# Optimization experiments

Measured on AMD Instinct MI355X. Metric: run time of the kernel, lower is better.

Reference implementation:

```python
import jax, jax.numpy as jnp
import numpy as np

HEADS = 4
K = 3  # neighborhood kernel size
EPS = 1e-5


def _nbr_idx(dim, k):
    # NATTEN semantics: window start clamped so the full k-window stays in-bounds.
    i = jnp.arange(dim)
    start = jnp.clip(i - k // 2, 0, dim - k)
    return start[:, None] + jnp.arange(k)[None, :]  # [dim, k]


def _gather_windows(t, ix, iy, iz):
    # t: [B, X, Y, Z, n, c] -> [B, X, Y, Z, K^3, n, c]
    t = t[:, ix]                 # [B, X, k, Y, Z, n, c]
    t = t[:, :, :, iy]           # [B, X, k, Y, k, Z, n, c]
    t = t[:, :, :, :, :, iz]     # [B, X, k, Y, k, Z, k, n, c]
    t = t.transpose(0, 1, 3, 5, 2, 4, 6, 7, 8)  # [B,X,Y,Z,k,k,k,n,c]
    B, X, Y, Z = t.shape[0], t.shape[1], t.shape[2], t.shape[3]
    return t.reshape(B, X, Y, Z, K * K * K, HEADS, -1)


def setup_inputs() -> dict:
    key = jax.random.key(0)
    k1, k2, k3 = jax.random.split(key, 3)
    C = 128
    x = jax.random.normal(k1, (1, C, 32, 32, 32), dtype=jnp.float32)
    ln_gamma = jnp.ones((C,), jnp.float32)
    ln_beta = jnp.zeros((C,), jnp.float32)
    qkv_w = jax.random.normal(k2, (3 * C, C), dtype=jnp.float32) * 0.02
    qkv_b = jnp.zeros((3 * C,), jnp.float32)
    proj_w = jax.random.normal(k3, (C, C), dtype=jnp.float32) * 0.02
    proj_b = jnp.zeros((C,), jnp.float32)
    return {"x": x, "ln_gamma": ln_gamma, "ln_beta": ln_beta,
            "qkv_w": qkv_w, "qkv_b": qkv_b, "proj_w": proj_w, "proj_b": proj_b}


def reference(x, ln_gamma, ln_beta, qkv_w, qkv_b, proj_w, proj_b):
    B, C, X, Y, Z = x.shape
    hd = C // HEADS
    scale = hd ** -0.5

    # permute to channels-last + LayerNorm over C
    h = x.transpose(0, 2, 3, 4, 1)  # [B,X,Y,Z,C]
    mu = jnp.mean(h, axis=-1, keepdims=True)
    var = jnp.mean(jnp.square(h - mu), axis=-1, keepdims=True)
    h = (h - mu) * jax.lax.rsqrt(var + EPS) * ln_gamma + ln_beta

    # QKV projection
    qkv = h @ qkv_w.T + qkv_b                     # [B,X,Y,Z,3C]
    q, k, v = jnp.split(qkv, 3, axis=-1)
    q = q.reshape(B, X, Y, Z, HEADS, hd)
    k = k.reshape(B, X, Y, Z, HEADS, hd)
    v = v.reshape(B, X, Y, Z, HEADS, hd)

    ix, iy, iz = _nbr_idx(X, K), _nbr_idx(Y, K), _nbr_idx(Z, K)
    k_win = _gather_windows(k, ix, iy, iz)  # [B,X,Y,Z,27,n,hd]
    v_win = _gather_windows(v, ix, iy, iz)

    attn = jnp.einsum('bxyznc,bxyzknc->bxyznk', q * scale, k_win)
    attn = jax.nn.softmax(attn, axis=-1)
    out = jnp.einsum('bxyznk,bxyzknc->bxyznc', attn, v_win)
    out = out.reshape(B, X, Y, Z, C)

    out = out @ proj_w.T + proj_b                 # output projection
    return out.transpose(0, 4, 1, 2, 3) + x      # residual, channels-first
```

## Files before the change

### kernel.cpp

```cpp
#include <hip/hip_runtime.h>

#define N_VOX 32768
#define CCH 128
#define EPSV 1e-5f

typedef __attribute__((ext_vector_type(8))) short bfrag;
typedef __attribute__((ext_vector_type(4))) float ffrag;
typedef __attribute__((ext_vector_type(2))) unsigned int u32x2;

__device__ __forceinline__ float bf2f(unsigned short u) {
    union { unsigned int i; float f; } c; c.i = ((unsigned int)u) << 16; return c.f;
}
__device__ __forceinline__ unsigned short f2bf(float f) {
    union { float f; unsigned int i; } c; c.f = f;
    unsigned int i = c.i;
    return (unsigned short)((i + 0x7FFFu + ((i >> 16) & 1u)) >> 16);
}
__device__ __forceinline__ unsigned int cvtpk(float lo, float hi) {
    unsigned int r;
    asm("v_cvt_pk_bf16_f32 %0, %1, %2" : "=v"(r) : "v"(lo), "v"(hi));
    return r;
}

__global__ __launch_bounds__(256) void ln_kernel(const float* __restrict__ x,
                                                 const float* __restrict__ gamma,
                                                 const float* __restrict__ beta,
                                                 unsigned short* __restrict__ h) {
    __shared__ float xs[128 * 65];
    __shared__ float g[128], b[128];
    __shared__ float ps[256], pq[256];
    __shared__ float muS[64], rsS[64];
    int t = threadIdx.x;
    int v0 = blockIdx.x * 64;
    if (t < 128) { g[t] = gamma[t]; b[t] = beta[t]; }
    int vv = t & 63, cq = t >> 6;
    for (int cb = 0; cb < 32; cb++) {
        int c = cb * 4 + cq;
        xs[c * 65 + vv] = x[(size_t)c * N_VOX + v0 + vv];
    }
    __syncthreads();
    float s = 0.f, sq = 0.f;
    for (int i = 0; i < 32; i++) {
        float val = xs[(cq * 32 + i) * 65 + vv];
        s += val; sq += val * val;
    }
    ps[t] = s; pq[t] = sq;
    __syncthreads();
    if (t < 64) {
        float S = ps[t] + ps[t + 64] + ps[t + 128] + ps[t + 192];
        float Q = pq[t] + pq[t + 64] + pq[t + 128] + pq[t + 192];
        float mu = S * (1.0f / 128.0f);
        float var = Q * (1.0f / 128.0f) - mu * mu;
        muS[t] = mu; rsS[t] = rsqrtf(var + EPSV);
    }
    __syncthreads();
    int c8 = t & 15;
    for (int pass = 0; pass < 4; pass++) {
        int v = pass * 16 + (t >> 4);
        float mu = muS[v], rs = rsS[v];
        float val[8];
        #pragma unroll
        for (int i = 0; i < 8; i++) {
            int c = c8 * 8 + i;
            val[i] = (xs[c * 65 + v] - mu) * rs * g[c] + b[c];
        }
        uint4 q;
        q.x = cvtpk(val[0], val[1]);
        q.y = cvtpk(val[2], val[3]);
        q.z = cvtpk(val[4], val[5]);
        q.w = cvtpk(val[6], val[7]);
        *(uint4*)&h[(size_t)(v0 + v) * 128 + c8 * 8] = q;
    }
}

__global__ __launch_bounds__(256) void qkv_gemm(const unsigned short* __restrict__ h,
                                                const float* __restrict__ w,
                                                const float* __restrict__ bias,
                                                unsigned short* __restrict__ qkv) {
    __shared__ __align__(16) unsigned short a_s[64 * 136];
    __shared__ __align__(16) unsigned short b_s[64 * 136];
    int t = threadIdx.x;
    int m0 = blockIdx.x * 64, o0 = blockIdx.y * 64;
    {
        int r4 = t >> 4, c8 = t & 15;
        #pragma unroll
        for (int pass = 0; pass < 4; pass++) {
            int r = pass * 16 + r4;
            *(uint4*)&a_s[r * 136 + c8 * 8] =
                *(const uint4*)&h[(size_t)(m0 + r) * 128 + c8 * 8];
            float4 w0 = *(const float4*)&w[(size_t)(o0 + r) * 128 + c8 * 8];
            float4 w1 = *(const float4*)&w[(size_t)(o0 + r) * 128 + c8 * 8 + 4];
            uint4 q;
            q.x = cvtpk(w0.x, w0.y);
            q.y = cvtpk(w0.z, w0.w);
            q.z = cvtpk(w1.x, w1.y);
            q.w = cvtpk(w1.z, w1.w);
            *(uint4*)&b_s[r * 136 + c8 * 8] = q;
        }
    }
    __syncthreads();
    int wvi = t >> 6, lane = t & 63, m = lane & 15, quad = lane >> 4;
    ffrag acc[4] = {ffrag{0,0,0,0}, ffrag{0,0,0,0}, ffrag{0,0,0,0}, ffrag{0,0,0,0}};
    #pragma unroll
    for (int kk = 0; kk < 4; kk++) {
        bfrag a = *(bfrag*)&a_s[(wvi * 16 + m) * 136 + kk * 32 + quad * 8];
        #pragma unroll
        for (int nt = 0; nt < 4; nt++) {
            bfrag bb = *(bfrag*)&b_s[(nt * 16 + m) * 136 + kk * 32 + quad * 8];
            acc[nt] = __builtin_amdgcn_mfma_f32_16x16x32_bf16(a, bb, acc[nt], 0, 0, 0);
        }
    }
    bool isq = (o0 < 128);
    #pragma unroll
    for (int nt = 0; nt < 4; nt++) {
        int o = o0 + nt * 16 + m;
        float bs = bias[o];
        int sec = o >> 7;
        int oc = o & 127;
        unsigned short* dst = qkv + (size_t)sec * ((size_t)N_VOX * 128);
        #pragma unroll
        for (int r = 0; r < 4; r++) {
            int vg = m0 + wvi * 16 + quad * 4 + r;
            float val = acc[nt][r] + bs;
            if (isq) val *= 0.17677669529663687f;
            dst[(size_t)vg * 128 + oc] = f2bf(val);
        }
    }
}

#define VT_STRIDE 188
__global__ __launch_bounds__(256) void attn_kernel(const unsigned short* __restrict__ qb,
                                                   const unsigned short* __restrict__ kb,
                                                   const unsigned short* __restrict__ vb,
                                                   unsigned short* __restrict__ ob) {
    __shared__ unsigned int vjtab[176];
    __shared__ __align__(16) unsigned short vt[4][32 * VT_STRIDE];

    int t = threadIdx.x;
    int hw = blockIdx.x;
    int bidx = (hw & 7) * 256 + (hw >> 3);
    int zh = bidx & 1, yy = (bidx >> 1) & 31, xx = bidx >> 6;
    int z0 = zh << 4;
    int sx = min(max(xx - 1, 0), 29);
    int sy = min(max(yy - 1, 0), 29);
    int zr0 = min(max(z0 - 1, 0), 14);
    int vox0 = (xx << 10) + (yy << 5) + z0;

    if (t < 176) {
        int r = t < 162 ? t : 161;
        int rxy = r / 18;
        int rzv = r - rxy * 18;
        int ax = rxy / 3;
        int by = rxy - ax * 3;
        vjtab[t] = (unsigned)(((sx + ax) << 10) + ((sy + by) << 5) + (zr0 + rzv));
    }
    __syncthreads();

    int wave = t >> 6, lane = t & 63;
    int hq = lane >> 4;
    int m = lane & 15;
    int ch0 = wave * 32;

    unsigned short* vts = &vt[wave][0];
    {
        const int cp = m;
        #pragma unroll
        for (int u = 0; u < 11; u++) {
            int rb = u * 16 + hq * 4;
            unsigned int j0 = vjtab[rb + 0];
            unsigned int j1 = vjtab[rb + 1];
            unsigned int j2 = vjtab[rb + 2];
            unsigned int j3 = vjtab[rb + 3];
            unsigned int d0 = *(const unsigned int*)&vb[(size_t)j0 * 128 + ch0 + cp * 2];
            unsigned int d1 = *(const unsigned int*)&vb[(size_t)j1 * 128 + ch0 + cp * 2];
            unsigned int d2 = *(const unsigned int*)&vb[(size_t)j2 * 128 + ch0 + cp * 2];
            unsigned int d3 = *(const unsigned int*)&vb[(size_t)j3 * 128 + ch0 + cp * 2];
            if (u == 10) {
                if (rb + 0 >= 162) d0 = 0u;
                if (rb + 1 >= 162) d1 = 0u;
                if (rb + 2 >= 162) d2 = 0u;
                if (rb + 3 >= 162) d3 = 0u;
            }
            unsigned int lo01 = __builtin_amdgcn_perm(d1, d0, 0x05040100u);
            unsigned int lo23 = __builtin_amdgcn_perm(d3, d2, 0x05040100u);
            unsigned int hi01 = __builtin_amdgcn_perm(d1, d0, 0x07060302u);
            unsigned int hi23 = __builtin_amdgcn_perm(d3, d2, 0x07060302u);
            u32x2 wlo; wlo.x = lo01; wlo.y = lo23;
            u32x2 whi; whi.x = hi01; whi.y = hi23;
            *(u32x2*)&vts[(2 * cp) * VT_STRIDE + rb] = wlo;
            *(u32x2*)&vts[(2 * cp + 1) * VT_STRIDE + rb] = whi;
        }
    }

    bfrag qf = *(const bfrag*)&qb[(size_t)(vox0 + m) * 128 + ch0 + hq * 8];
    ffrag s[11];
    #pragma unroll
    for (int f = 0; f < 11; f++) {
        unsigned int vj = vjtab[f * 16 + m];
        bfrag kf = *(const bfrag*)&kb[(size_t)vj * 128 + ch0 + hq * 8];
        s[f] = __builtin_amdgcn_mfma_f32_16x16x32_bf16(kf, qf, ffrag{0,0,0,0}, 0, 0, 0);
    }

    int zv = z0 + m;
    int szv = min(max(zv - 1, 0), 29);
    unsigned int wz = (unsigned int)(szv - zr0);
    unsigned int rz = 4u * (unsigned int)hq;
    float mx = -1e30f;
    #pragma unroll
    for (int f = 0; f < 11; f++) {
        #pragma unroll
        for (int i = 0; i < 4; i++) {
            unsigned int ri = rz + (unsigned int)i;
            ri = min(ri, ri - 18u);
            bool valid = (ri - wz) <= 2u;
            if (f == 10) valid = valid && ((4 * hq + i) < 2);
            float sv = valid ? s[f][i] : -1e30f;
            s[f][i] = sv;
            mx = fmaxf(mx, sv);
        }
        rz = min(rz + 16u, rz - 2u);
    }
    mx = fmaxf(mx, __shfl_xor(mx, 16));
    mx = fmaxf(mx, __shfl_xor(mx, 32));
    float sum = 0.f;
    #pragma unroll
    for (int f = 0; f < 11; f++) {
        #pragma unroll
        for (int i = 0; i < 4; i++) {
            float p = __expf(s[f][i] - mx);
            s[f][i] = p;
            sum += p;
        }
    }
    sum += __shfl_xor(sum, 16);
    sum += __shfl_xor(sum, 32);
    float inv = 1.0f / sum;

    ffrag acc0 = ffrag{0,0,0,0};
    ffrag acc1 = ffrag{0,0,0,0};
    const unsigned short* ab = &vt[wave][m * VT_STRIDE + hq * 4];
    #pragma unroll
    for (int f = 0; f < 11; f++) {
        u32x2 pb; pb.x = cvtpk(s[f][0], s[f][1]); pb.y = cvtpk(s[f][2], s[f][3]);
        u32x2 av0 = *(const u32x2*)&ab[f * 16];
        u32x2 av1 = *(const u32x2*)&ab[16 * VT_STRIDE + f * 16];
        asm("v_mfma_f32_16x16x16_bf16 %0, %1, %2, %0" : "+v"(acc0) : "v"(av0), "v"(pb));
        asm("v_mfma_f32_16x16x16_bf16 %0, %1, %2, %0" : "+v"(acc1) : "v"(av1), "v"(pb));
    }

    size_t obase = (size_t)(vox0 + m) * 128 + ch0 + hq * 4;
    {
        u32x2 ov;
        ov.x = cvtpk(acc0[0] * inv, acc0[1] * inv);
        ov.y = cvtpk(acc0[2] * inv, acc0[3] * inv);
        *(u32x2*)&ob[obase] = ov;
    }
    {
        u32x2 ov;
        ov.x = cvtpk(acc1[0] * inv, acc1[1] * inv);
        ov.y = cvtpk(acc1[2] * inv, acc1[3] * inv);
        *(u32x2*)&ob[obase + 16] = ov;
    }
}

__global__ __launch_bounds__(256) void proj_gemm(const unsigned short* __restrict__ a,
                                                 const float* __restrict__ w,
                                                 const float* __restrict__ bias,
                                                 const float* __restrict__ xres,
                                                 float* __restrict__ out) {
    __shared__ __align__(16) unsigned short a_s[64 * 136];
    __shared__ __align__(16) unsigned short b_s[64 * 136];
    int t = threadIdx.x;
    int m0 = blockIdx.x * 64, o0 = blockIdx.y * 64;
    {
        int r4 = t >> 4, c8 = t & 15;
        #pragma unroll
        for (int pass = 0; pass < 4; pass++) {
            int r = pass * 16 + r4;
            *(uint4*)&a_s[r * 136 + c8 * 8] =
                *(const uint4*)&a[(size_t)(m0 + r) * 128 + c8 * 8];
            float4 w0 = *(const float4*)&w[(size_t)(o0 + r) * 128 + c8 * 8];
            float4 w1 = *(const float4*)&w[(size_t)(o0 + r) * 128 + c8 * 8 + 4];
            uint4 q;
            q.x = cvtpk(w0.x, w0.y);
            q.y = cvtpk(w0.z, w0.w);
            q.z = cvtpk(w1.x, w1.y);
            q.w = cvtpk(w1.z, w1.w);
            *(uint4*)&b_s[r * 136 + c8 * 8] = q;
        }
    }
    __syncthreads();
    int wvi = t >> 6, lane = t & 63, m = lane & 15, quad = lane >> 4;
    ffrag acc[4] = {ffrag{0,0,0,0}, ffrag{0,0,0,0}, ffrag{0,0,0,0}, ffrag{0,0,0,0}};
    #pragma unroll
    for (int kk = 0; kk < 4; kk++) {
        bfrag av = *(bfrag*)&a_s[(wvi * 16 + m) * 136 + kk * 32 + quad * 8];
        #pragma unroll
        for (int nt = 0; nt < 4; nt++) {
            bfrag bb = *(bfrag*)&b_s[(nt * 16 + m) * 136 + kk * 32 + quad * 8];
            acc[nt] = __builtin_amdgcn_mfma_f32_16x16x32_bf16(av, bb, acc[nt], 0, 0, 0);
        }
    }
    #pragma unroll
    for (int nt = 0; nt < 4; nt++) {
        int o = o0 + nt * 16 + m;
        float bs = bias[o];
        int vg = m0 + wvi * 16 + quad * 4;
        float4 r = *(const float4*)&xres[(size_t)o * N_VOX + vg];
        float4 ov;
        ov.x = acc[nt][0] + bs + r.x;
        ov.y = acc[nt][1] + bs + r.y;
        ov.z = acc[nt][2] + bs + r.z;
        ov.w = acc[nt][3] + bs + r.w;
        *(float4*)&out[(size_t)o * N_VOX + vg] = ov;
    }
}

extern "C" void kernel_launch(void* const* d_in, const int* in_sizes, int n_in,
                              void* d_out, int out_size, void* d_ws, size_t ws_size,
                              hipStream_t stream) {
    const float* x      = (const float*)d_in[0];
    const float* gamma  = (const float*)d_in[1];
    const float* beta   = (const float*)d_in[2];
    const float* qkv_w  = (const float*)d_in[3];
    const float* qkv_b  = (const float*)d_in[4];
    const float* proj_w = (const float*)d_in[5];
    const float* proj_b = (const float*)d_in[6];
    float* out = (float*)d_out;

    unsigned short* h    = (unsigned short*)d_ws;
    unsigned short* qkv  = (unsigned short*)((char*)d_ws + (8u << 20));
    unsigned short* attn = h;

    hipLaunchKernelGGL(ln_kernel, dim3(512), dim3(256), 0, stream, x, gamma, beta, h);
    hipLaunchKernelGGL(qkv_gemm, dim3(512, 6), dim3(256), 0, stream, h, qkv_w, qkv_b, qkv);
    const unsigned short* qb = qkv;
    const unsigned short* kb = qkv + (size_t)N_VOX * 128;
    const unsigned short* vb = qkv + (size_t)2 * N_VOX * 128;
    hipLaunchKernelGGL(attn_kernel, dim3(2048), dim3(256), 0, stream, qb, kb, vb, attn);
    hipLaunchKernelGGL(proj_gemm, dim3(512, 2), dim3(256), 0, stream, attn, proj_w, proj_b, x, out);
}
```

Measured before the change: 119.8 us.

## Fuse LayerNorm into QKV GEMM, recomputing LN per output-column group

Merges the LayerNorm kernel and the QKV projection into one kernel. Each block normalizes 64 voxels straight from x into shared memory as bf16, keeps the A fragments in registers, and loops over three 64-wide weight tiles to cover 192 output channels. This removes the bf16 h intermediate round trip and one launch. In exchange, each 64-voxel LN tile is recomputed twice (two output groups), per-block serial work grows, and the grid shrinks from 3072 to 1024 blocks.

After: 118.2 us. Within noise of the previous version (-1.3%).

```diff
diff --git a/kernel.cpp b/kernel.cpp
--- a/kernel.cpp
+++ b/kernel.cpp
@@ -22,27 +22,28 @@
     return r;
 }
 
-__global__ __launch_bounds__(256) void ln_kernel(const float* __restrict__ x,
-                                                 const float* __restrict__ gamma,
-                                                 const float* __restrict__ beta,
-                                                 unsigned short* __restrict__ h) {
-    __shared__ float xs[128 * 65];
-    __shared__ float g[128], b[128];
+__global__ __launch_bounds__(256) void ln_qkv(const float* __restrict__ x,
+                                              const float* __restrict__ gamma,
+                                              const float* __restrict__ beta,
+                                              const float* __restrict__ w,
+                                              const float* __restrict__ bias,
+                                              unsigned short* __restrict__ qkv) {
+    __shared__ __align__(16) unsigned short a_s[64 * 136];
+    __shared__ __align__(16) unsigned short b_s[64 * 136];
     __shared__ float ps[256], pq[256];
     __shared__ float muS[64], rsS[64];
+    __shared__ float g[128], bta[128];
     int t = threadIdx.x;
-    int v0 = blockIdx.x * 64;
-    if (t < 128) { g[t] = gamma[t]; b[t] = beta[t]; }
-    int vv = t & 63, cq = t >> 6;
-    for (int cb = 0; cb < 32; cb++) {
-        int c = cb * 4 + cq;
-        xs[c * 65 + vv] = x[(size_t)c * N_VOX + v0 + vv];
-    }
-    __syncthreads();
+    int og = blockIdx.x;
+    int v0 = blockIdx.y * 64;
+    if (t < 128) { g[t] = gamma[t]; bta[t] = beta[t]; }
+    int cq = t >> 6, v = t & 63;
+    float xr[32];
     float s = 0.f, sq = 0.f;
+    #pragma unroll
     for (int i = 0; i < 32; i++) {
-        float val = xs[(cq * 32 + i) * 65 + vv];
-        s += val; sq += val * val;
+        float val = x[(size_t)(cq * 32 + i) * N_VOX + v0 + v];
+        xr[i] = val; s += val; sq += val * val;
     }
     ps[t] = s; pq[t] = sq;
     __syncthreads();
@@ -54,77 +55,74 @@
         muS[t] = mu; rsS[t] = rsqrtf(var + EPSV);
     }
     __syncthreads();
-    int c8 = t & 15;
-    for (int pass = 0; pass < 4; pass++) {
-        int v = pass * 16 + (t >> 4);
+    {
         float mu = muS[v], rs = rsS[v];
-        float val[8];
-        #pragma unroll
-        for (int i = 0; i < 8; i++) {
-            int c = c8 * 8 + i;
-            val[i] = (xs[c * 65 + v] - mu) * rs * g[c] + b[c];
-        }
-        uint4 q;
-        q.x = cvtpk(val[0], val[1]);
-        q.y = cvtpk(val[2], val[3]);
-        q.z = cvtpk(val[4], val[5]);
-        q.w = cvtpk(val[6], val[7]);
-        *(uint4*)&h[(size_t)(v0 + v) * 128 + c8 * 8] = q;
-    }
-}
-
-__global__ __launch_bounds__(256) void qkv_gemm(const unsigned short* __restrict__ h,
-                                                const float* __restrict__ w,
-                                                const float* __restrict__ bias,
-                                                unsigned short* __restrict__ qkv) {
-    __shared__ __align__(16) unsigned short a_s[64 * 136];
-    __shared__ __align__(16) unsigned short b_s[64 * 136];
-    int t = threadIdx.x;
-    int m0 = blockIdx.x * 64, o0 = blockIdx.y * 64;
-    {
-        int r4 = t >> 4, c8 = t & 15;
-        #pragma unroll
-        for (int pass = 0; pass < 4; pass++) {
-            int r = pass * 16 + r4;
-            *(uint4*)&a_s[r * 136 + c8 * 8] =
-                *(const uint4*)&h[(size_t)(m0 + r) * 128 + c8 * 8];
-            float4 w0 = *(const float4*)&w[(size_t)(o0 + r) * 128 + c8 * 8];
-            float4 w1 = *(const float4*)&w[(size_t)(o0 + r) * 128 + c8 * 8 + 4];
+        #pragma unroll
+        for (int i8 = 0; i8 < 4; i8++) {
+            float val[8];
+            #pragma unroll
+            for (int k = 0; k < 8; k++) {
+                int c = cq * 32 + i8 * 8 + k;
+                val[k] = (xr[i8 * 8 + k] - mu) * rs * g[c] + bta[c];
+            }
             uint4 q;
-            q.x = cvtpk(w0.x, w0.y);
-            q.y = cvtpk(w0.z, w0.w);
-            q.z = cvtpk(w1.x, w1.y);
-            q.w = cvtpk(w1.z, w1.w);
-            *(uint4*)&b_s[r * 136 + c8 * 8] = q;
-        }
-    }
-    __syncthreads();
-    int wvi = t >> 6, lane = t & 63, m = lane & 15, quad = lane >> 4;
-    ffrag acc[4] = {ffrag{0,0,0,0}, ffrag{0,0,0,0}, ffrag{0,0,0,0}, ffrag{0,0,0,0}};
-    #pragma unroll
-    for (int kk = 0; kk < 4; kk++) {
-        bfrag a = *(bfrag*)&a_s[(wvi * 16 + m) * 136 + kk * 32 + quad * 8];
+            q.x = cvtpk(val[0], val[1]);
+            q.y = cvtpk(val[2], val[3]);
+            q.z = cvtpk(val[4], val[5]);
+            q.w = cvtpk(val[6], val[7]);
+            *(uint4*)&a_s[v * 136 + cq * 32 + i8 * 8] = q;
+        }
+    }
+    __syncthreads();
+    int lane = t & 63, wvi = t >> 6, m = lane & 15, quad = lane >> 4;
+    bfrag areg[4];
+    #pragma unroll
+    for (int kk = 0; kk < 4; kk++)
+        areg[kk] = *(bfrag*)&a_s[(wvi * 16 + m) * 136 + kk * 32 + quad * 8];
+    for (int t0 = 0; t0 < 3; t0++) {
+        int o0 = og * 192 + t0 * 64;
+        {
+            int r4 = t >> 4, c8 = t & 15;
+            #pragma unroll
+            for (int pass = 0; pass < 4; pass++) {
+                int r = pass * 16 + r4;
+                float4 w0 = *(const float4*)&w[(size_t)(o0 + r) * 128 + c8 * 8];
+                float4 w1 = *(const float4*)&w[(size_t)(o0 + r) * 128 + c8 * 8 + 4];
+                uint4 q;
+                q.x = cvtpk(w0.x, w0.y);
+                q.y = cvtpk(w0.z, w0.w);
+                q.z = cvtpk(w1.x, w1.y);
+                q.w = cvtpk(w1.z, w1.w);
+                *(uint4*)&b_s[r * 136 + c8 * 8] = q;
+            }
+        }
+        __syncthreads();
+        ffrag acc[4] = {ffrag{0,0,0,0}, ffrag{0,0,0,0}, ffrag{0,0,0,0}, ffrag{0,0,0,0}};
+        #pragma unroll
+        for (int kk = 0; kk < 4; kk++) {
+            #pragma unroll
+            for (int nt = 0; nt < 4; nt++) {
+                bfrag bb = *(bfrag*)&b_s[(nt * 16 + m) * 136 + kk * 32 + quad * 8];
+                acc[nt] = __builtin_amdgcn_mfma_f32_16x16x32_bf16(areg[kk], bb, acc[nt], 0, 0, 0);
+            }
+        }
+        bool isq = (o0 < 128);
         #pragma unroll
         for (int nt = 0; nt < 4; nt++) {
-            bfrag bb = *(bfrag*)&b_s[(nt * 16 + m) * 136 + kk * 32 + quad * 8];
-            acc[nt] = __builtin_amdgcn_mfma_f32_16x16x32_bf16(a, bb, acc[nt], 0, 0, 0);
-        }
-    }
-    bool isq = (o0 < 128);
-    #pragma unroll
-    for (int nt = 0; nt < 4; nt++) {
-        int o = o0 + nt * 16 + m;
-        float bs = bias[o];
-        int sec = o >> 7;
-        int oc = o & 127;
-        unsigned short* dst = qkv + (size_t)sec * ((size_t)N_VOX * 128);
-        #pragma unroll
-        for (int r = 0; r < 4; r++) {
-            int vg = m0 + wvi * 16 + quad * 4 + r;
-            float val = acc[nt][r] + bs;
-            if (isq) val *= 0.17677669529663687f;
-            dst[(size_t)vg * 128 + oc] = f2bf(val);
-        }
+            int o = o0 + nt * 16 + m;
+            float bs = bias[o];
+            int sec = o >> 7;
+            int oc = o & 127;
+            unsigned short* dst = qkv + (size_t)sec * ((size_t)N_VOX * 128);
+            #pragma unroll
+            for (int r = 0; r < 4; r++) {
+                int vg = v0 + wvi * 16 + quad * 4 + r;
+                float val = acc[nt][r] + bs;
+                if (isq) val *= 0.17677669529663687f;
+                dst[(size_t)vg * 128 + oc] = f2bf(val);
+            }
+        }
+        __syncthreads();
     }
 }
 
@@ -328,12 +326,11 @@
     const float* proj_b = (const float*)d_in[6];
     float* out = (float*)d_out;
 
-    unsigned short* h    = (unsigned short*)d_ws;
-    unsigned short* qkv  = (unsigned short*)((char*)d_ws + (8u << 20));
-    unsigned short* attn = h;
-
-    hipLaunchKernelGGL(ln_kernel, dim3(512), dim3(256), 0, stream, x, gamma, beta, h);
-    hipLaunchKernelGGL(qkv_gemm, dim3(512, 6), dim3(256), 0, stream, h, qkv_w, qkv_b, qkv);
+    unsigned short* qkv  = (unsigned short*)d_ws;
+    unsigned short* attn = (unsigned short*)((char*)d_ws + (24u << 20));
+
+    hipLaunchKernelGGL(ln_qkv, dim3(2, 512), dim3(256), 0, stream,
+                       x, gamma, beta, qkv_w, qkv_b, qkv);
     const unsigned short* qb = qkv;
     const unsigned short* kb = qkv + (size_t)N_VOX * 128;
     const unsigned short* vb = qkv + (size_t)2 * N_VOX * 128;
```
